# Kernel tuning notes

Hardware: AMD Instinct MI355X
Metric: run time of the kernel (lower is better)

## Reference

```python
import jax, jax.numpy as jnp
import numpy as np

TAU = 2.0
HEADS = 8

@jax.custom_vjp
def heaviside(x):
    return (x >= 0).astype(x.dtype)

def _hv_fwd(x):
    return (x >= 0).astype(x.dtype), x

def _hv_bwd(x, g):
    # spikingjelly default surrogate: sigmoid, alpha=4
    s = jax.nn.sigmoid(4.0 * x)
    return (g * 4.0 * s * (1.0 - s),)

heaviside.defvjp(_hv_fwd, _hv_bwd)

def lif(x, v_th=1.0):
    # MultiStepLIFNode(tau=2, v_reset=0, detach_reset, hard reset); x: [T, ...]
    def step(v, xt):
        v = v + (xt - v) / TAU
        s = heaviside(v - v_th)
        v = v * (1.0 - jax.lax.stop_gradient(s))
        return v, s
    _, spikes = jax.lax.scan(step, jnp.zeros_like(x[0]), x)
    return spikes

def bn_c(x, p, eps=1e-5):
    # eval-mode BatchNorm over channel axis 2; p rows: gamma, beta, mean, var
    sh = [1] * x.ndim
    sh[2] = p.shape[1]
    g, b, m, v = (p[i].reshape(sh) for i in range(4))
    return g * (x - m) * jax.lax.rsqrt(v + eps) + b

def setup_inputs():
    key = jax.random.key(0)
    ks = jax.random.split(key, 17)
    T, B, C, H, W = 4, 16, 256, 32, 32
    Hd = 4 * C
    f = lambda k, sh, sc: jax.random.normal(k, sh, jnp.float32) * sc
    u = lambda k, sh: jax.random.uniform(k, sh, jnp.float32)
    return {
        "x": f(ks[0], (T, B, C, H, W), 1.0),
        "res_attn": jnp.zeros((1,), jnp.float32),
        "wq": f(ks[1], (C, C), C ** -0.5),
        "bn_q": u(ks[2], (4, C)),
        "wk": f(ks[3], (C, C), C ** -0.5),
        "bn_k": u(ks[4], (4, C)),
        "wv": f(ks[5], (C, C), C ** -0.5),
        "bn_v": u(ks[6], (4, C)),
        "w_proj": f(ks[7], (C, C), C ** -0.5),
        "b_proj": f(ks[8], (C,), 0.02),
        "bn_proj": u(ks[9], (4, C)),
        "w_fc1": f(ks[10], (Hd, C), C ** -0.5),
        "b_fc1": f(ks[11], (Hd,), 0.02),
        "bn_fc1": u(ks[12], (4, Hd)),
        "w_fc2": f(ks[13], (C, Hd), Hd ** -0.5),
        "b_fc2": f(ks[14], (C,), 0.02),
        "bn_fc2": u(ks[15], (4, C)),
    }

def reference(x, res_attn, wq, bn_q, wk, bn_k, wv, bn_v, w_proj, b_proj, bn_proj,
              w_fc1, b_fc1, bn_fc1, w_fc2, b_fc2, bn_fc2):
    T, B, C, H, W = x.shape
    N = H * W
    d = C // HEADS
    scale = 0.125
    xf = x.reshape(T, B, C, N)

    def qkv(w, bnp):
        y = jnp.einsum('oc,tbcn->tbon', w, xf)  # conv1x1, no bias
        return lif(bn_c(y, bnp))

    # [T,B,C,N] -> [T,B,h,N,d]; channel c = h*d + di (matches torch reshape)
    to_heads = lambda t: t.reshape(T, B, HEADS, d, N).transpose(0, 1, 2, 4, 3)
    q = to_heads(qkv(wq, bn_q))
    k = to_heads(qkv(wk, bn_k))
    v = to_heads(qkv(wv, bn_v))

    kv = jnp.einsum('tbhnd,tbhne->tbhde', k, v)          # [T,B,h,d,d]
    a = jnp.einsum('tbhnd,tbhde->tbhne', q, kv) * scale  # [T,B,h,N,d]
    a = a.transpose(0, 1, 2, 4, 3).reshape(T, B, C, N)   # transpose(3,4)+reshape
    a = lif(a, v_th=0.5)                                 # attn_lif

    p = jnp.einsum('oc,tbcn->tbon', w_proj, a) + b_proj[None, None, :, None]
    attn_out = lif(bn_c(p, bn_proj).reshape(T, B, C, H, W))

    x = x + attn_out

    h1 = jnp.einsum('oc,tbchw->tbohw', w_fc1, x) + b_fc1[None, None, :, None, None]
    h1 = lif(bn_c(h1, bn_fc1))
    h2 = jnp.einsum('co,tbohw->tbchw', w_fc2, h1) + b_fc2[None, None, :, None, None]
    mlp_out = lif(bn_c(h2, bn_fc2))

    return x + mlp_out
```

## Files before the change

kernel.cpp:

```cpp
#include <hip/hip_runtime.h>
#include <stdint.h>
#include <math.h>

#define T_ 4
#define B_ 16
#define C_ 256
#define N_ 1024
#define HD_ 1024
#define HEADS_ 8
#define DH_ 32

typedef float v2f  __attribute__((ext_vector_type(2)));
typedef float f4v  __attribute__((ext_vector_type(4)));
typedef float f16v __attribute__((ext_vector_type(16)));

#define PKLs(a, w, x) asm volatile("v_pk_fma_f32 %0, %1, %2, %0 op_sel:[0,0,0] op_sel_hi:[0,1,1]" : "+v"(a) : "s"(w), "v"(x))
#define PKHs(a, w, x) asm volatile("v_pk_fma_f32 %0, %1, %2, %0 op_sel:[1,0,0] op_sel_hi:[1,1,1]" : "+v"(a) : "s"(w), "v"(x))

__device__ __forceinline__ void drainl(){
  asm volatile("s_waitcnt lgkmcnt(0)" ::: "memory");
  __builtin_amdgcn_sched_barrier(0);
}

__global__ __launch_bounds__(256)
void packW(const float* __restrict__ W, float* __restrict__ Wp,
           int K, int OD, int ooff)
{
  int k = blockIdx.x*256 + threadIdx.x;
  int oo = blockIdx.y + ooff;
  Wp[((size_t)(k>>1)*(OD>>3) + (oo>>3))*16 + ((k&1)<<3) + (oo&7)]
      = W[(size_t)blockIdx.y*K + k];
}

__global__ __launch_bounds__(256)
void packBn3(const float* __restrict__ a, const float* __restrict__ b,
             const float* __restrict__ c, float* __restrict__ o)
{
  int i = blockIdx.x*256 + threadIdx.x;
  int r = i >> 8, ci = i & 255;
  o[(size_t)r*768 + ci]       = a[i];
  o[(size_t)r*768 + 256 + ci] = b[i];
  o[(size_t)r*768 + 512 + ci] = c[i];
}

template<typename T> struct VecT;
template<> struct VecT<float>  { using t = float4; };
template<> struct VecT<uint8_t>{ using t = uchar4; };
__device__ __forceinline__ float4 cvt4(float4 v){ return v; }
__device__ __forceinline__ float4 cvt4(uchar4 u){
  return make_float4((float)u.x,(float)u.y,(float)u.z,(float)u.w);
}

template<int KDIM,int ODIM,bool HAS_BIAS,int MODE,typename TIn>
__global__ __launch_bounds__(256,3)
void sgemm(const TIn* __restrict__ X, const float* __restrict__ Wp,
           const float* __restrict__ bias, const float* __restrict__ bn,
           const float* __restrict__ resid, void* __restrict__ out, float vth)
{
  using XV = typename VecT<TIn>::t;
  constexpr int NC = KDIM/16;
  __shared__ __align__(16) float Xs[2][16*256];

  const int tid  = threadIdx.x;
  const int lane = tid & 63;
  const int wid  = __builtin_amdgcn_readfirstlane(tid >> 6);
  const int b    = blockIdx.z, n0 = blockIdx.x*256, o0 = blockIdx.y*32;
  const int og   = (o0 >> 3) + wid;
  const uint32_t laB =
      (uint32_t)(uintptr_t)(__attribute__((address_space(3))) float*)&Xs[0][0]
      + (uint32_t)(lane*16);

  v2f acc[8][2], vli[8][2];
#pragma unroll
  for (int i=0;i<8;i++){ vli[i][0]=(v2f){0.f,0.f}; vli[i][1]=(v2f){0.f,0.f}; }

  union WU { f16v v; v2f p[8]; };
  WU wbuf[2];
  f4v xbuf[2][2];
  XV  sreg[4];

  auto ldstage = [&](int ch){
    const int t = ch / NC, c = ch % NC;
    const TIn* Xg = X + ((size_t)(t*B_+b)*KDIM + c*16)*N_ + n0 + (tid&63)*4;
#pragma unroll
    for (int r=0;r<4;r++)
      sreg[r] = *(const XV*)(Xg + (size_t)((tid>>6) + 4*r)*N_);
  };

#define ISSUEH(pb, c, h) do{                                                   \
    const float* wp_ = Wp + ((size_t)((c)*8 + (h))*(ODIM>>3) + og)*16;         \
    asm volatile("s_load_dwordx16 %0, %1, 0x0"                                 \
                 : "=s"(wbuf[(h)&1].v) : "s"(wp_));                            \
    uint32_t la_ = laB + (uint32_t)((pb)*16384 + (h)*2048);                    \
    asm volatile("ds_read_b128 %0, %2\n\tds_read_b128 %1, %2 offset:1024"      \
                 : "=v"(xbuf[(h)&1][0]), "=v"(xbuf[(h)&1][1]) : "v"(la_));     \
  }while(0)

#define CH(h) do{                                                              \
    _Pragma("unroll")                                                          \
    for (int e=0;e<2;e++){                                                     \
      v2f xa = __builtin_shufflevector(xbuf[(h)&1][e], xbuf[(h)&1][e], 0,1);   \
      v2f xc = __builtin_shufflevector(xbuf[(h)&1][e], xbuf[(h)&1][e], 2,3);   \
      _Pragma("unroll")                                                        \
      for (int j=0;j<4;j++){                                                   \
        PKLs(acc[2*j  ][0], wbuf[(h)&1].p[4*e+j], xa);                         \
        PKLs(acc[2*j  ][1], wbuf[(h)&1].p[4*e+j], xc);                         \
        PKHs(acc[2*j+1][0], wbuf[(h)&1].p[4*e+j], xa);                         \
        PKHs(acc[2*j+1][1], wbuf[(h)&1].p[4*e+j], xc);                         \
      }                                                                        \
    } }while(0)

#define CHUNK(pb, t, c) do{                                                    \
    __syncthreads();                                                           \
    _Pragma("unroll")                                                          \
    for (int r=0;r<4;r++)                                                      \
      *(float4*)&Xs[pb][((tid>>6) + 4*r)*256 + (tid&63)*4] = cvt4(sreg[r]);    \
    __syncthreads();                                                           \
    { int nch = (t)*NC + (c) + 1; if (nch < T_*NC) ldstage(nch); }             \
    ISSUEH(pb,c,0);                                                            \
    drainl(); ISSUEH(pb,c,1); CH(0);                                           \
    drainl(); ISSUEH(pb,c,2); CH(1);                                           \
    drainl(); ISSUEH(pb,c,3); CH(2);                                           \
    drainl(); ISSUEH(pb,c,4); CH(3);                                           \
    drainl(); ISSUEH(pb,c,5); CH(4);                                           \
    drainl(); ISSUEH(pb,c,6); CH(5);                                           \
    drainl(); ISSUEH(pb,c,7); CH(6);                                           \
    drainl(); CH(7);                                                           \
  }while(0)

  ldstage(0);

  for (int t=0;t<T_;t++){
#pragma unroll
    for (int i=0;i<8;i++){ acc[i][0]=(v2f){0.f,0.f}; acc[i][1]=(v2f){0.f,0.f}; }

#pragma unroll 1
    for (int cc=0; cc<NC; cc+=2){
      CHUNK(0, t, cc);
      CHUNK(1, t, cc+1);
    }

#pragma unroll
    for (int i=0;i<8;i++){
      const int o = o0 + wid*8 + i;
      const float g  = bn[o];
      const float be = bn[ODIM + o];
      const float m  = bn[2*ODIM + o];
      const float rs = 1.0f / sqrtf(bn[3*ODIM + o] + 1e-5f);
      const float bi = HAS_BIAS ? bias[o] : 0.0f;
      float sv[4];
#pragma unroll
      for (int jj=0;jj<4;jj++){
        float y  = acc[i][jj>>1][jj&1] + bi;
        float yb = (g*(y - m))*rs + be;
        float vv = vli[i][jj>>1][jj&1];
        vv += (yb - vv)*0.5f;
        float s = (vv >= vth) ? 1.0f : 0.0f;
        vli[i][jj>>1][jj&1] = (s!=0.0f) ? 0.0f : vv;
        sv[jj] = s;
      }
      const size_t base = ((size_t)(t*B_+b)*ODIM + o)*N_ + n0 + 4*lane;
      if (MODE==0){
        uchar4 pa;
        pa.x=(uint8_t)sv[0]; pa.y=(uint8_t)sv[1]; pa.z=(uint8_t)sv[2]; pa.w=(uint8_t)sv[3];
        *(uchar4*)((uint8_t*)out + base) = pa;
      } else {
        const float4 r0 = *(const float4*)&resid[base];
        *(float4*)&((float*)out)[base] =
          make_float4(r0.x+sv[0], r0.y+sv[1], r0.z+sv[2], r0.w+sv[3]);
      }
    }
  }
#undef ISSUEH
#undef CH
#undef CHUNK
}

__global__ __launch_bounds__(256)
void kv_kernel(const uint8_t* __restrict__ qkv, float* __restrict__ kvout)
{
  int blk = blockIdx.x;
  int h = blk & 7, tb = blk >> 3;
  int tid = threadIdx.x;
  int e = tid & 31, d0 = (tid >> 5) * 4;
  const uint8_t* kp = qkv + ((size_t)tb*768 + 256 + h*DH_)*N_;
  const uint8_t* vp = qkv + ((size_t)tb*768 + 512 + h*DH_)*N_;
  const uint4* vr = (const uint4*)(vp + (size_t)e*N_);
  const uint4* k0 = (const uint4*)(kp + (size_t)(d0+0)*N_);
  const uint4* k1 = (const uint4*)(kp + (size_t)(d0+1)*N_);
  const uint4* k2 = (const uint4*)(kp + (size_t)(d0+2)*N_);
  const uint4* k3 = (const uint4*)(kp + (size_t)(d0+3)*N_);
  int s0=0,s1=0,s2=0,s3=0;
  for (int q=0;q<N_/16;q++){
    uint4 vv = vr[q];
    uint4 a0 = k0[q], a1 = k1[q], a2 = k2[q], a3 = k3[q];
    s0 += __popc(a0.x&vv.x)+__popc(a0.y&vv.y)+__popc(a0.z&vv.z)+__popc(a0.w&vv.w);
    s1 += __popc(a1.x&vv.x)+__popc(a1.y&vv.y)+__popc(a1.z&vv.z)+__popc(a1.w&vv.w);
    s2 += __popc(a2.x&vv.x)+__popc(a2.y&vv.y)+__popc(a2.z&vv.z)+__popc(a2.w&vv.w);
    s3 += __popc(a3.x&vv.x)+__popc(a3.y&vv.y)+__popc(a3.z&vv.z)+__popc(a3.w&vv.w);
  }
  float* kvp = kvout + (size_t)blk*DH_*DH_;
  kvp[(d0+0)*DH_ + e] = (float)s0;
  kvp[(d0+1)*DH_ + e] = (float)s1;
  kvp[(d0+2)*DH_ + e] = (float)s2;
  kvp[(d0+3)*DH_ + e] = (float)s3;
}

__global__ __launch_bounds__(256)
void attn_lif_kernel(const uint8_t* __restrict__ qkv, const float* __restrict__ kv,
                     uint8_t* __restrict__ as_)
{
  int tid = threadIdx.x;
  int n = blockIdx.x*256 + tid;
  int h = blockIdx.y, b = blockIdx.z;
  __shared__ float kvL[DH_*DH_];
  float v[DH_];
#pragma unroll
  for (int e=0;e<DH_;e++) v[e]=0.0f;
  for (int t=0;t<T_;t++){
    const float* kvp = kv + ((size_t)((t*B_+b)*HEADS_+h))*DH_*DH_;
    __syncthreads();
#pragma unroll
    for (int r=0;r<4;r++) kvL[tid+256*r] = kvp[tid+256*r];
    __syncthreads();
    const uint8_t* qp = qkv + ((size_t)(t*B_+b)*768 + h*DH_)*N_ + n;
    float qv[DH_];
#pragma unroll
    for (int d=0;d<DH_;d++) qv[d] = (float)qp[(size_t)d*N_];
    uint8_t* op = as_ + ((size_t)(t*B_+b)*C_ + h*DH_)*N_ + n;
#pragma unroll
    for (int e=0;e<DH_;e++){
      float a=0.0f;
#pragma unroll
      for (int d=0;d<DH_;d++) a += qv[d]*kvL[d*DH_+e];
      a *= 0.125f;
      float vv = v[e];
      vv += (a - vv)*0.5f;
      float s = (vv >= 0.5f) ? 1.0f : 0.0f;
      v[e] = (s!=0.0f) ? 0.0f : vv;
      op[(size_t)e*N_] = (uint8_t)s;
    }
  }
}

extern "C" void kernel_launch(void* const* d_in, const int* in_sizes, int n_in,
                              void* d_out, int out_size, void* d_ws, size_t ws_size,
                              hipStream_t stream)
{
  const float* x      = (const float*)d_in[0];
  const float* wq     = (const float*)d_in[2];
  const float* bn_q   = (const float*)d_in[3];
  const float* wk     = (const float*)d_in[4];
  const float* bn_k   = (const float*)d_in[5];
  const float* wv     = (const float*)d_in[6];
  const float* bn_v   = (const float*)d_in[7];
  const float* wproj  = (const float*)d_in[8];
  const float* bproj  = (const float*)d_in[9];
  const float* bnproj = (const float*)d_in[10];
  const float* wfc1   = (const float*)d_in[11];
  const float* bfc1   = (const float*)d_in[12];
  const float* bnfc1  = (const float*)d_in[13];
  const float* wfc2   = (const float*)d_in[14];
  const float* bfc2   = (const float*)d_in[15];
  const float* bnfc2  = (const float*)d_in[16];

  char* ws = (char*)d_ws;
  const size_t TB = (size_t)T_*B_;
  uint8_t* qkv = (uint8_t*)ws;
  uint8_t* as_ = (uint8_t*)ws + TB*768*N_;
  uint8_t* h1s = (uint8_t*)ws;
  size_t off = TB*768*N_ + TB*(size_t)C_*N_;
  float* xnew = (float*)(ws + off); off += TB*(size_t)C_*N_*4;
  float* WpQ  = (float*)(ws + off); off += (size_t)C_*768*4;
  float* WpP  = (float*)(ws + off); off += (size_t)C_*C_*4;
  float* WpF1 = (float*)(ws + off); off += (size_t)C_*HD_*4;
  float* WpF2 = (float*)(ws + off); off += (size_t)HD_*C_*4;
  float* bnQ  = (float*)(ws + off); off += 4*768*4;
  float* kvb  = (float*)(ws + off); off += TB*HEADS_*DH_*DH_*4;

  dim3 blk(256);
  packW<<<dim3(1,256),blk,0,stream>>>(wq,    WpQ,  256,  768,   0);
  packW<<<dim3(1,256),blk,0,stream>>>(wk,    WpQ,  256,  768, 256);
  packW<<<dim3(1,256),blk,0,stream>>>(wv,    WpQ,  256,  768, 512);
  packW<<<dim3(1,256),blk,0,stream>>>(wproj, WpP,  256,  256,   0);
  packW<<<dim3(1,1024),blk,0,stream>>>(wfc1, WpF1, 256, 1024,   0);
  packW<<<dim3(4,256),blk,0,stream>>>(wfc2,  WpF2, 1024, 256,   0);
  packBn3<<<dim3(4),blk,0,stream>>>(bn_q, bn_k, bn_v, bnQ);

  sgemm<C_,768,false,0,float><<<dim3(4,24,16),blk,0,stream>>>(
      x, WpQ, nullptr, bnQ, nullptr, qkv, 1.0f);
  kv_kernel<<<dim3(T_*B_*HEADS_),blk,0,stream>>>(qkv, kvb);
  attn_lif_kernel<<<dim3(4,HEADS_,B_),blk,0,stream>>>(qkv, kvb, as_);
  sgemm<C_,C_,true,1,uint8_t><<<dim3(4,8,16),blk,0,stream>>>(
      as_, WpP, bproj, bnproj, x, xnew, 1.0f);
  sgemm<C_,HD_,true,0,float><<<dim3(4,32,16),blk,0,stream>>>(
      xnew, WpF1, bfc1, bnfc1, nullptr, h1s, 1.0f);
  sgemm<HD_,C_,true,1,uint8_t><<<dim3(4,8,16),blk,0,stream>>>(
      h1s, WpF2, bfc2, bnfc2, xnew, d_out, 1.0f);
}
```

Baseline: 1.462 ms.

## Stage GEMM weights through LDS instead of scalar loads, with partial waitcnt

```diff
diff --git a/kernel.cpp b/kernel.cpp
--- a/kernel.cpp
+++ b/kernel.cpp
@@ -10,15 +10,15 @@
 #define HEADS_ 8
 #define DH_ 32
 
-typedef float v2f  __attribute__((ext_vector_type(2)));
-typedef float f4v  __attribute__((ext_vector_type(4)));
-typedef float f16v __attribute__((ext_vector_type(16)));
-
-#define PKLs(a, w, x) asm volatile("v_pk_fma_f32 %0, %1, %2, %0 op_sel:[0,0,0] op_sel_hi:[0,1,1]" : "+v"(a) : "s"(w), "v"(x))
-#define PKHs(a, w, x) asm volatile("v_pk_fma_f32 %0, %1, %2, %0 op_sel:[1,0,0] op_sel_hi:[1,1,1]" : "+v"(a) : "s"(w), "v"(x))
-
-__device__ __forceinline__ void drainl(){
-  asm volatile("s_waitcnt lgkmcnt(0)" ::: "memory");
+typedef float   v2f  __attribute__((ext_vector_type(2)));
+typedef float   f4v  __attribute__((ext_vector_type(4)));
+typedef uint8_t u8x4 __attribute__((ext_vector_type(4)));
+
+#define PKL(a, w, x) asm volatile("v_pk_fma_f32 %0, %1, %2, %0 op_sel:[0,0,0] op_sel_hi:[0,1,1]" : "+v"(a) : "v"(w), "v"(x))
+#define PKH(a, w, x) asm volatile("v_pk_fma_f32 %0, %1, %2, %0 op_sel:[1,0,0] op_sel_hi:[1,1,1]" : "+v"(a) : "v"(w), "v"(x))
+
+template<int N> __device__ __forceinline__ void waitl(){
+  asm volatile("s_waitcnt lgkmcnt(%0)" :: "i"(N) : "memory");
   __builtin_amdgcn_sched_barrier(0);
 }
 
@@ -44,88 +44,106 @@
 }
 
 template<typename T> struct VecT;
-template<> struct VecT<float>  { using t = float4; };
-template<> struct VecT<uint8_t>{ using t = uchar4; };
-__device__ __forceinline__ float4 cvt4(float4 v){ return v; }
-__device__ __forceinline__ float4 cvt4(uchar4 u){
-  return make_float4((float)u.x,(float)u.y,(float)u.z,(float)u.w);
+template<> struct VecT<float>  { using t = f4v;  };
+template<> struct VecT<uint8_t>{ using t = u8x4; };
+__device__ __forceinline__ f4v cvt4(f4v v){ return v; }
+__device__ __forceinline__ f4v cvt4(u8x4 u){
+  return (f4v){ (float)u[0], (float)u[1], (float)u[2], (float)u[3] };
 }
 
 template<int KDIM,int ODIM,bool HAS_BIAS,int MODE,typename TIn>
 __global__ __launch_bounds__(256,3)
-void sgemm(const TIn* __restrict__ X, const float* __restrict__ Wp,
+void dgemm(const TIn* __restrict__ X, const float* __restrict__ Wp,
            const float* __restrict__ bias, const float* __restrict__ bn,
            const float* __restrict__ resid, void* __restrict__ out, float vth)
 {
   using XV = typename VecT<TIn>::t;
   constexpr int NC = KDIM/16;
   __shared__ __align__(16) float Xs[2][16*256];
+  __shared__ __align__(16) float Ws[2][512];
 
   const int tid  = threadIdx.x;
   const int lane = tid & 63;
   const int wid  = __builtin_amdgcn_readfirstlane(tid >> 6);
   const int b    = blockIdx.z, n0 = blockIdx.x*256, o0 = blockIdx.y*32;
-  const int og   = (o0 >> 3) + wid;
-  const uint32_t laB =
+  const int og0  = o0 >> 3;
+  const int wh = tid >> 5, wg = (tid >> 3) & 3, we = tid & 7;
+
+  const uint32_t lxB =
       (uint32_t)(uintptr_t)(__attribute__((address_space(3))) float*)&Xs[0][0]
       + (uint32_t)(lane*16);
+  const uint32_t lwB =
+      (uint32_t)(uintptr_t)(__attribute__((address_space(3))) float*)&Ws[0][0]
+      + (uint32_t)(wid*64);
 
   v2f acc[8][2], vli[8][2];
 #pragma unroll
   for (int i=0;i<8;i++){ vli[i][0]=(v2f){0.f,0.f}; vli[i][1]=(v2f){0.f,0.f}; }
 
-  union WU { f16v v; v2f p[8]; };
-  WU wbuf[2];
-  f4v xbuf[2][2];
+  f4v xb[2][2];
+  f4v wrg[2][4];
   XV  sreg[4];
+  v2f wsreg;
 
   auto ldstage = [&](int ch){
     const int t = ch / NC, c = ch % NC;
-    const TIn* Xg = X + ((size_t)(t*B_+b)*KDIM + c*16)*N_ + n0 + (tid&63)*4;
+    const TIn* Xg = X + ((size_t)(t*B_+b)*KDIM + c*16)*N_ + n0 + lane*4;
 #pragma unroll
     for (int r=0;r<4;r++)
-      sreg[r] = *(const XV*)(Xg + (size_t)((tid>>6) + 4*r)*N_);
+      sreg[r] = *(const __attribute__((address_space(1))) XV*)
+                  (Xg + (size_t)((tid>>6) + 4*r)*N_);
+    wsreg = *(const __attribute__((address_space(1))) v2f*)
+        (Wp + ((size_t)(c*8 + wh)*(ODIM>>3) + og0 + wg)*16 + 2*we);
   };
 
-#define ISSUEH(pb, c, h) do{                                                   \
-    const float* wp_ = Wp + ((size_t)((c)*8 + (h))*(ODIM>>3) + og)*16;         \
-    asm volatile("s_load_dwordx16 %0, %1, 0x0"                                 \
-                 : "=s"(wbuf[(h)&1].v) : "s"(wp_));                            \
-    uint32_t la_ = laB + (uint32_t)((pb)*16384 + (h)*2048);                    \
+#define ISSUEH(pb, h) do{                                                      \
+    uint32_t lx_ = lxB + (uint32_t)((pb)*16384 + (h)*2048);                    \
     asm volatile("ds_read_b128 %0, %2\n\tds_read_b128 %1, %2 offset:1024"      \
-                 : "=v"(xbuf[(h)&1][0]), "=v"(xbuf[(h)&1][1]) : "v"(la_));     \
+                 : "=v"(xb[(h)&1][0]), "=v"(xb[(h)&1][1]) : "v"(lx_));         \
+    uint32_t lw_ = lwB + (uint32_t)((pb)*2048 + (h)*256);                      \
+    asm volatile("ds_read_b128 %0, %4\n\tds_read_b128 %1, %4 offset:16\n\t"    \
+                 "ds_read_b128 %2, %4 offset:32\n\tds_read_b128 %3, %4 offset:48" \
+                 : "=v"(wrg[(h)&1][0]), "=v"(wrg[(h)&1][1]),                   \
+                   "=v"(wrg[(h)&1][2]), "=v"(wrg[(h)&1][3]) : "v"(lw_));       \
   }while(0)
 
 #define CH(h) do{                                                              \
     _Pragma("unroll")                                                          \
     for (int e=0;e<2;e++){                                                     \
-      v2f xa = __builtin_shufflevector(xbuf[(h)&1][e], xbuf[(h)&1][e], 0,1);   \
-      v2f xc = __builtin_shufflevector(xbuf[(h)&1][e], xbuf[(h)&1][e], 2,3);   \
-      _Pragma("unroll")                                                        \
-      for (int j=0;j<4;j++){                                                   \
-        PKLs(acc[2*j  ][0], wbuf[(h)&1].p[4*e+j], xa);                         \
-        PKLs(acc[2*j  ][1], wbuf[(h)&1].p[4*e+j], xc);                         \
-        PKHs(acc[2*j+1][0], wbuf[(h)&1].p[4*e+j], xa);                         \
-        PKHs(acc[2*j+1][1], wbuf[(h)&1].p[4*e+j], xc);                         \
-      }                                                                        \
+      v2f xa = __builtin_shufflevector(xb[(h)&1][e], xb[(h)&1][e], 0,1);       \
+      v2f xc = __builtin_shufflevector(xb[(h)&1][e], xb[(h)&1][e], 2,3);       \
+      f4v A = wrg[(h)&1][2*e], Bv = wrg[(h)&1][2*e+1];                         \
+      v2f wa = __builtin_shufflevector(A,A,0,1);                               \
+      v2f wb2= __builtin_shufflevector(A,A,2,3);                               \
+      v2f wc = __builtin_shufflevector(Bv,Bv,0,1);                             \
+      v2f wd = __builtin_shufflevector(Bv,Bv,2,3);                             \
+      PKL(acc[0][0],wa,xa);  PKL(acc[0][1],wa,xc);                             \
+      PKH(acc[1][0],wa,xa);  PKH(acc[1][1],wa,xc);                             \
+      PKL(acc[2][0],wb2,xa); PKL(acc[2][1],wb2,xc);                            \
+      PKH(acc[3][0],wb2,xa); PKH(acc[3][1],wb2,xc);                            \
+      PKL(acc[4][0],wc,xa);  PKL(acc[4][1],wc,xc);                             \
+      PKH(acc[5][0],wc,xa);  PKH(acc[5][1],wc,xc);                             \
+      PKL(acc[6][0],wd,xa);  PKL(acc[6][1],wd,xc);                             \
+      PKH(acc[7][0],wd,xa);  PKH(acc[7][1],wd,xc);                             \
     } }while(0)
 
 #define CHUNK(pb, t, c) do{                                                    \
     __syncthreads();                                                           \
     _Pragma("unroll")                                                          \
     for (int r=0;r<4;r++)                                                      \
-      *(float4*)&Xs[pb][((tid>>6) + 4*r)*256 + (tid&63)*4] = cvt4(sreg[r]);    \
+      *(f4v*)&Xs[pb][((tid>>6) + 4*r)*256 + lane*4] = cvt4(sreg[r]);           \
+    *(v2f*)&Ws[pb][(wh*4+wg)*16 + 2*we] = wsreg;                               \
     __syncthreads();                                                           \
     { int nch = (t)*NC + (c) + 1; if (nch < T_*NC) ldstage(nch); }             \
-    ISSUEH(pb,c,0);                                                            \
-    drainl(); ISSUEH(pb,c,1); CH(0);                                           \
-    drainl(); ISSUEH(pb,c,2); CH(1);                                           \
-    drainl(); ISSUEH(pb,c,3); CH(2);                                           \
-    drainl(); ISSUEH(pb,c,4); CH(3);                                           \
-    drainl(); ISSUEH(pb,c,5); CH(4);                                           \
-    drainl(); ISSUEH(pb,c,6); CH(5);                                           \
-    drainl(); ISSUEH(pb,c,7); CH(6);                                           \
-    drainl(); CH(7);                                                           \
+    ISSUEH(pb,0);                                                              \
+    ISSUEH(pb,1); waitl<6>(); CH(0);                                           \
+    ISSUEH(pb,2); waitl<6>(); CH(1);                                           \
+    ISSUEH(pb,3); waitl<6>(); CH(2);                                           \
+    ISSUEH(pb,4); waitl<6>(); CH(3);                                           \
+    ISSUEH(pb,5); waitl<6>(); CH(4);                                           \
+    ISSUEH(pb,6); waitl<6>(); CH(5);                                           \
+    ISSUEH(pb,7); waitl<6>(); CH(6);                                           \
+    waitl<0>(); CH(7);                                                         \
   }while(0)
 
   ldstage(0);
@@ -161,13 +179,12 @@
       }
       const size_t base = ((size_t)(t*B_+b)*ODIM + o)*N_ + n0 + 4*lane;
       if (MODE==0){
-        uchar4 pa;
-        pa.x=(uint8_t)sv[0]; pa.y=(uint8_t)sv[1]; pa.z=(uint8_t)sv[2]; pa.w=(uint8_t)sv[3];
-        *(uchar4*)((uint8_t*)out + base) = pa;
+        u8x4 pa = { (uint8_t)sv[0], (uint8_t)sv[1], (uint8_t)sv[2], (uint8_t)sv[3] };
+        *(u8x4*)((uint8_t*)out + base) = pa;
       } else {
-        const float4 r0 = *(const float4*)&resid[base];
-        *(float4*)&((float*)out)[base] =
-          make_float4(r0.x+sv[0], r0.y+sv[1], r0.z+sv[2], r0.w+sv[3]);
+        f4v r0 = *(const f4v*)&resid[base];
+        f4v w0 = { r0[0]+sv[0], r0[1]+sv[1], r0[2]+sv[2], r0[3]+sv[3] };
+        *(f4v*)&((float*)out)[base] = w0;
       }
     }
   }
@@ -287,14 +304,14 @@
   packW<<<dim3(4,256),blk,0,stream>>>(wfc2,  WpF2, 1024, 256,   0);
   packBn3<<<dim3(4),blk,0,stream>>>(bn_q, bn_k, bn_v, bnQ);
 
-  sgemm<C_,768,false,0,float><<<dim3(4,24,16),blk,0,stream>>>(
+  dgemm<C_,768,false,0,float><<<dim3(4,24,16),blk,0,stream>>>(
       x, WpQ, nullptr, bnQ, nullptr, qkv, 1.0f);
   kv_kernel<<<dim3(T_*B_*HEADS_),blk,0,stream>>>(qkv, kvb);
   attn_lif_kernel<<<dim3(4,HEADS_,B_),blk,0,stream>>>(qkv, kvb, as_);
-  sgemm<C_,C_,true,1,uint8_t><<<dim3(4,8,16),blk,0,stream>>>(
+  dgemm<C_,C_,true,1,uint8_t><<<dim3(4,8,16),blk,0,stream>>>(
       as_, WpP, bproj, bnproj, x, xnew, 1.0f);
-  sgemm<C_,HD_,true,0,float><<<dim3(4,32,16),blk,0,stream>>>(
+  dgemm<C_,HD_,true,0,float><<<dim3(4,32,16),blk,0,stream>>>(
       xnew, WpF1, bfc1, bnfc1, nullptr, h1s, 1.0f);
-  sgemm<HD_,C_,true,1,uint8_t><<<dim3(4,8,16),blk,0,stream>>>(
+  dgemm<HD_,C_,true,1,uint8_t><<<dim3(4,8,16),blk,0,stream>>>(
       h1s, WpF2, bfc2, bnfc2, xnew, d_out, 1.0f);
 }
```

After: 1.477 ms. About the same (+1.0%).
